# Kernel tuning notes

Hardware: AMD Instinct MI355X
Metric: run time of the kernel (lower is better)

The kernel has to match this reference:

```python
import jax, jax.numpy as jnp
import numpy as np

B, Q, K, D = 8, 2048, 2048, 64

def setup_inputs() -> dict:
    key = jax.random.key(0)
    kq, kk, kv, kl = jax.random.split(key, 4)
    queries = jax.random.normal(kq, (B, Q, D), dtype=jnp.float32)
    keys = jax.random.normal(kk, (B, K, D), dtype=jnp.float32)
    values = jax.random.normal(kv, (B, K, D), dtype=jnp.float32)
    valid_lens = jax.random.randint(kl, (B,), 1, K + 1)  # at least 1 valid key
    return {"queries": queries, "keys": keys, "values": values, "valid_lens": valid_lens}

def reference(queries, keys, values, valid_lens):
    d = queries.shape[-1]
    # scores: [B, Q, K]
    scores = jnp.einsum("bqd,bkd->bqk", queries, keys) / jnp.sqrt(jnp.float32(d))
    # d2l-style masked softmax: positions >= valid_len get -1e6 before softmax
    kpos = jnp.arange(scores.shape[-1])  # [K]
    mask = kpos[None, None, :] < valid_lens[:, None, None]  # [B,1,K]
    scores = jnp.where(mask, scores, jnp.float32(-1e6))
    attn = jax.nn.softmax(scores, axis=-1)
    # dropout is identity at inference (training=False)
    return jnp.einsum("bqk,bkd->bqd", attn, values)
```

## Files before the change

### kernel.cpp

```cpp
#include <hip/hip_runtime.h>

typedef float    f32x4  __attribute__((ext_vector_type(4)));
typedef float    f32x16 __attribute__((ext_vector_type(16)));
typedef _Float16 half8  __attribute__((ext_vector_type(8)));

constexpr int NB = 8;
constexpr int NQ = 2048;
constexpr int NKEY = 2048;
constexpr int DD = 64;
constexpr int KB = 64;

#define QSCALE (0.125f * 1.44269504088896340736f)

__device__ inline unsigned pkh(float a, float b) {
    return __builtin_bit_cast(unsigned, __builtin_amdgcn_cvt_pkrtz(a, b));
}
__device__ inline int vswz(int d) {
    return (((d >> 3) & 3) | ((d & 1) << 2)) << 4;
}

__device__ __forceinline__ void pv_chunk(
    const f32x16& sv, const char* __restrict__ vsm, int koff,
    int hi, int ql, int swzq, f32x16& o0, f32x16& o1)
{
    const unsigned w0 = pkh(sv[0],  sv[1]),  w1 = pkh(sv[2],  sv[3]);
    const unsigned w2 = pkh(sv[4],  sv[5]),  w3 = pkh(sv[6],  sv[7]);
    const unsigned w4 = pkh(sv[8],  sv[9]),  w5 = pkh(sv[10], sv[11]);
    const unsigned w6 = pkh(sv[12], sv[13]), w7 = pkh(sv[14], sv[15]);
    const unsigned p0 = __shfl_xor(w0, 32), p1 = __shfl_xor(w1, 32);
    const unsigned p2 = __shfl_xor(w2, 32), p3 = __shfl_xor(w3, 32);
    const unsigned p4 = __shfl_xor(w4, 32), p5 = __shfl_xor(w5, 32);
    const unsigned p6 = __shfl_xor(w6, 32), p7 = __shfl_xor(w7, 32);
    const bool h1 = (hi != 0);
    union { unsigned u[4]; half8 h; } A0, A1;
    A0.u[0] = h1 ? p2 : w0;  A0.u[1] = h1 ? p3 : w1;
    A0.u[2] = h1 ? w2 : p0;  A0.u[3] = h1 ? w3 : p1;
    A1.u[0] = h1 ? p6 : w4;  A1.u[1] = h1 ? p7 : w5;
    A1.u[2] = h1 ? w6 : p4;  A1.u[3] = h1 ? w7 : p5;

#pragma unroll
    for (int t = 0; t < 2; ++t) {
        const int co = koff + t * 32 + hi * 16;
        const half8 vb0 = *(const half8*)(vsm + ql * 128        + (co ^ swzq));
        const half8 vb1 = *(const half8*)(vsm + (32 + ql) * 128 + (co ^ swzq));
        const half8 pa = (t == 0) ? A0.h : A1.h;
        o0 = __builtin_amdgcn_mfma_f32_32x32x16_f16(pa, vb0, o0, 0, 0, 0);
        o1 = __builtin_amdgcn_mfma_f32_32x32x16_f16(pa, vb1, o1, 0, 0, 0);
    }
}

__global__ __launch_bounds__(256, 2) void attn_fused(
    const float* __restrict__ Qp, const float* __restrict__ Kp,
    const float* __restrict__ Vp, const int* __restrict__ VL,
    float* __restrict__ Op)
{
    __shared__ __align__(16) char pool[65536];

    const int tid  = threadIdx.x;
    const int wv   = tid >> 6;
    const int lane = tid & 63;
    const int ql   = lane & 31;
    const int hi   = lane >> 5;

    char* Ksm = pool + wv * 16384;
    char* Vsm = Ksm + 8192;

    const int b  = blockIdx.x & 7;
    const int qt = blockIdx.x >> 3;
    const int qbase = qt * 32;

    const int vlen = VL[b];
    const int numt = (vlen + KB - 1) / KB;

    const float* qsrc = Qp + ((size_t)b * NQ + qbase + ql) * DD;
    half8 qf[4];
#pragma unroll
    for (int c = 0; c < 4; ++c) {
        f32x4 f0 = *(const f32x4*)(qsrc + c * 16 + hi * 8);
        f32x4 f1 = *(const f32x4*)(qsrc + c * 16 + hi * 8 + 4);
        half8 h;
#pragma unroll
        for (int j = 0; j < 4; ++j) {
            h[j]     = (_Float16)(f0[j] * QSCALE);
            h[4 + j] = (_Float16)(f1[j] * QSCALE);
        }
        qf[c] = h;
    }

    f32x16 o0 = {}, o1 = {};
    float mrun = -1e30f, lrun = 0.f;

    const int kr_ = lane >> 3;
    const int kd0 = (lane & 7) * 8;
    const int vk2 = (lane >> 4) * 2;
    const int vd0 = (lane & 15) * 4;
    const int swzq = vswz(ql);

    for (int t = wv; t < numt; t += 4) {
        const int kbase = t * KB;
        const float* kbp = Kp + ((size_t)b * NKEY + kbase) * DD;
        const float* vbp = Vp + ((size_t)b * NKEY + kbase) * DD;

        f32x4 ka[8][2];
#pragma unroll
        for (int i = 0; i < 8; ++i) {
            const float* src = kbp + (size_t)(i * 8 + kr_) * DD + kd0;
            ka[i][0] = *(const f32x4*)src;
            ka[i][1] = *(const f32x4*)(src + 4);
        }
        f32x4 va[8][2];
#pragma unroll
        for (int i = 0; i < 8; ++i) {
            const float* src = vbp + (size_t)(i * 8 + vk2) * DD + vd0;
            va[i][0] = *(const f32x4*)src;
            va[i][1] = *(const f32x4*)(src + DD);
        }

#pragma unroll
        for (int i = 0; i < 8; ++i) {
            half8 h;
#pragma unroll
            for (int j = 0; j < 4; ++j) {
                h[j]     = (_Float16)ka[i][0][j];
                h[4 + j] = (_Float16)ka[i][1][j];
            }
            const int off = ((i * 8 + kr_) * 128 + kd0 * 2) ^ (kr_ << 4);
            *(half8*)(Ksm + off) = h;
        }

        f32x16 svA = {}, svB = {};
#pragma unroll
        for (int c = 0; c < 4; ++c) {
            const half8 kfA = *(const half8*)(Ksm +
                ((ql * 128 + c * 32 + hi * 16) ^ ((ql & 7) << 4)));
            svA = __builtin_amdgcn_mfma_f32_32x32x16_f16(kfA, qf[c], svA, 0, 0, 0);
            const half8 kfB = *(const half8*)(Ksm +
                (((32 + ql) * 128 + c * 32 + hi * 16) ^ ((ql & 7) << 4)));
            svB = __builtin_amdgcn_mfma_f32_32x32x16_f16(kfB, qf[c], svB, 0, 0, 0);
        }

#pragma unroll
        for (int i = 0; i < 8; ++i) {
#pragma unroll
            for (int jj = 0; jj < 4; ++jj) {
                const int d = vd0 + jj;
                const unsigned w = pkh(va[i][0][jj], va[i][1][jj]);
                *(unsigned*)(Vsm + d * 128 + (((i * 16 + vk2 * 2)) ^ vswz(d))) = w;
            }
        }

        if (kbase + KB > vlen) {
#pragma unroll
            for (int r = 0; r < 16; ++r) {
                const int krow = (r & 3) + 8 * (r >> 2) + 4 * hi;
                svA[r] = (kbase + krow < vlen)      ? svA[r] : -1e30f;
                svB[r] = (kbase + 32 + krow < vlen) ? svB[r] : -1e30f;
            }
        }

        float mx[16];
#pragma unroll
        for (int r = 0; r < 16; ++r) mx[r] = fmaxf(svA[r], svB[r]);
#pragma unroll
        for (int st = 8; st > 0; st >>= 1)
#pragma unroll
            for (int r = 0; r < st; ++r) mx[r] = fmaxf(mx[r], mx[r + st]);
        float mr = fmaxf(mx[0], __shfl_xor(mx[0], 32));

        if (!__all(mr <= mrun + 8.f)) {
            const float mn = fmaxf(mrun, mr);
            const float alpha = __builtin_amdgcn_exp2f(mrun - mn);
            lrun *= alpha;
            mrun = mn;
#pragma unroll
            for (int r = 0; r < 16; ++r) {
                const int qr = (r & 3) + 8 * (r >> 2) + 4 * hi;
                const float ar = __shfl(alpha, qr);
                o0[r] *= ar;
                o1[r] *= ar;
            }
        }

#pragma unroll
        for (int r = 0; r < 16; ++r) {
            svA[r] = __builtin_amdgcn_exp2f(svA[r] - mrun);
            svB[r] = __builtin_amdgcn_exp2f(svB[r] - mrun);
        }
        float sx[16];
#pragma unroll
        for (int r = 0; r < 16; ++r) sx[r] = svA[r] + svB[r];
#pragma unroll
        for (int st = 8; st > 0; st >>= 1)
#pragma unroll
            for (int r = 0; r < st; ++r) sx[r] += sx[r + st];
        lrun += sx[0] + __shfl_xor(sx[0], 32);

        pv_chunk(svA, Vsm, 0,  hi, ql, swzq, o0, o1);
        pv_chunk(svB, Vsm, 64, hi, ql, swzq, o0, o1);
    }

    __syncthreads();
    float* Mb = (float*)(pool + 32768);
    float* Lb = (float*)(pool + 32768 + 512);
    float* Tb = (float*)(pool + 32768 + 1024);
    float (*Obuf)[32][64] = (float (*)[32][64])pool;

    if (hi == 0) { Mb[wv * 32 + ql] = mrun; Lb[wv * 32 + ql] = lrun; }
    __syncthreads();

    float Mtot = -1e30f;
#pragma unroll
    for (int w = 0; w < 4; ++w)
        if (Lb[w * 32 + ql] > 0.f) Mtot = fmaxf(Mtot, Mb[w * 32 + ql]);
    float Ltot = 0.f;
#pragma unroll
    for (int w = 0; w < 4; ++w) {
        const float lw = Lb[w * 32 + ql];
        if (lw > 0.f) Ltot += lw * __builtin_amdgcn_exp2f(Mb[w * 32 + ql] - Mtot);
    }
    const float wown = (lrun > 0.f) ? __builtin_amdgcn_exp2f(mrun - Mtot) : 0.f;
    if (wv == 0 && hi == 0) Tb[ql] = Ltot;

#pragma unroll
    for (int r = 0; r < 16; ++r) {
        const int qr = (r & 3) + 8 * (r >> 2) + 4 * hi;
        const float wr = __shfl(wown, qr);
        Obuf[wv][qr][ql]      = o0[r] * wr;
        Obuf[wv][qr][ql + 32] = o1[r] * wr;
    }
    __syncthreads();

#pragma unroll
    for (int k = 0; k < 8; ++k) {
        const int q = wv * 8 + k;
        const float sum = Obuf[0][q][lane] + Obuf[1][q][lane]
                        + Obuf[2][q][lane] + Obuf[3][q][lane];
        Op[((size_t)b * NQ + qbase + q) * DD + lane] = sum / Tb[q];
    }
}

extern "C" void kernel_launch(void* const* d_in, const int* in_sizes, int n_in,
                              void* d_out, int out_size, void* d_ws, size_t ws_size,
                              hipStream_t stream) {
    const float* Qp = (const float*)d_in[0];
    const float* Kp = (const float*)d_in[1];
    const float* Vp = (const float*)d_in[2];
    const int*   VL = (const int*)d_in[3];
    float* Op = (float*)d_out;

    dim3 block(256);
    dim3 grid(NB * (NQ / 32));
    hipLaunchKernelGGL(attn_fused, grid, block, 0, stream, Qp, Kp, Vp, VL, Op);
}
```

Before: 30.29 us.

## Prefetch next K tile into registers, add MFMA priority, remap block-to-batch order

Restructures the per-wave key loop into a software pipeline. The next K tile (t+4) is loaded from global into a second register buffer while the current tile is converted and used, with the loop unrolled by two to ping-pong the buffers. It also raises wave priority around the MFMA sections with s_setprio, and changes the blockIdx mapping so neighbouring blocks interleave batches in groups of 8. The aim is to hide global load latency and improve MFMA issue. The risk is higher register pressure from the extra 32-float buffer, which could cause spills or reduce occupancy under launch_bounds(256,2).

```diff
diff --git a/kernel.cpp b/kernel.cpp
--- a/kernel.cpp
+++ b/kernel.cpp
@@ -38,6 +38,7 @@
     A1.u[0] = h1 ? p6 : w4;  A1.u[1] = h1 ? p7 : w5;
     A1.u[2] = h1 ? w6 : p4;  A1.u[3] = h1 ? w7 : p5;
 
+    __builtin_amdgcn_s_setprio(1);
 #pragma unroll
     for (int t = 0; t < 2; ++t) {
         const int co = koff + t * 32 + hi * 16;
@@ -47,6 +48,125 @@
         o0 = __builtin_amdgcn_mfma_f32_32x32x16_f16(pa, vb0, o0, 0, 0, 0);
         o1 = __builtin_amdgcn_mfma_f32_32x32x16_f16(pa, vb1, o1, 0, 0, 0);
     }
+    __builtin_amdgcn_s_setprio(0);
+}
+
+__device__ __forceinline__ void load_k(
+    f32x4 (&ka)[8][2], const float* __restrict__ kbp, int kr_, int kd0)
+{
+#pragma unroll
+    for (int i = 0; i < 8; ++i) {
+        const float* src = kbp + (size_t)(i * 8 + kr_) * DD + kd0;
+        ka[i][0] = *(const f32x4*)src;
+        ka[i][1] = *(const f32x4*)(src + 4);
+    }
+}
+
+__device__ __forceinline__ void iter_body(
+    f32x4 (&ka)[8][2], f32x4 (&kan)[8][2],
+    int t, int numt, int vlen, int b,
+    const float* __restrict__ Kp, const float* __restrict__ Vp,
+    char* __restrict__ Ksm, char* __restrict__ Vsm,
+    int ql, int hi, int kr_, int kd0, int vk2, int vd0, int swzq,
+    const half8 (&qf)[4], f32x16& o0, f32x16& o1, float& mrun, float& lrun)
+{
+    const int kbase = t * KB;
+
+    f32x4 va[8][2];
+    const float* vbp = Vp + ((size_t)b * NKEY + kbase) * DD;
+#pragma unroll
+    for (int i = 0; i < 8; ++i) {
+        const float* src = vbp + (size_t)(i * 8 + vk2) * DD + vd0;
+        va[i][0] = *(const f32x4*)src;
+        va[i][1] = *(const f32x4*)(src + DD);
+    }
+
+#pragma unroll
+    for (int i = 0; i < 8; ++i) {
+        half8 h;
+#pragma unroll
+        for (int j = 0; j < 4; ++j) {
+            h[j]     = (_Float16)ka[i][0][j];
+            h[4 + j] = (_Float16)ka[i][1][j];
+        }
+        const int off = ((i * 8 + kr_) * 128 + kd0 * 2) ^ (kr_ << 4);
+        *(half8*)(Ksm + off) = h;
+    }
+
+    if (t + 4 < numt)
+        load_k(kan, Kp + ((size_t)b * NKEY + (t + 4) * KB) * DD, kr_, kd0);
+
+    f32x16 svA = {}, svB = {};
+    __builtin_amdgcn_s_setprio(1);
+#pragma unroll
+    for (int c = 0; c < 4; ++c) {
+        const half8 kfA = *(const half8*)(Ksm +
+            ((ql * 128 + c * 32 + hi * 16) ^ ((ql & 7) << 4)));
+        svA = __builtin_amdgcn_mfma_f32_32x32x16_f16(kfA, qf[c], svA, 0, 0, 0);
+        const half8 kfB = *(const half8*)(Ksm +
+            (((32 + ql) * 128 + c * 32 + hi * 16) ^ ((ql & 7) << 4)));
+        svB = __builtin_amdgcn_mfma_f32_32x32x16_f16(kfB, qf[c], svB, 0, 0, 0);
+    }
+    __builtin_amdgcn_s_setprio(0);
+
+#pragma unroll
+    for (int i = 0; i < 8; ++i) {
+#pragma unroll
+        for (int jj = 0; jj < 4; ++jj) {
+            const int d = vd0 + jj;
+            const unsigned w = pkh(va[i][0][jj], va[i][1][jj]);
+            *(unsigned*)(Vsm + d * 128 + ((i * 16 + vk2 * 2) ^ vswz(d))) = w;
+        }
+    }
+
+    if (kbase + KB > vlen) {
+#pragma unroll
+        for (int r = 0; r < 16; ++r) {
+            const int krow = (r & 3) + 8 * (r >> 2) + 4 * hi;
+            svA[r] = (kbase + krow < vlen)      ? svA[r] : -1e30f;
+            svB[r] = (kbase + 32 + krow < vlen) ? svB[r] : -1e30f;
+        }
+    }
+
+    float mx[16];
+#pragma unroll
+    for (int r = 0; r < 16; ++r) mx[r] = fmaxf(svA[r], svB[r]);
+#pragma unroll
+    for (int st = 8; st > 0; st >>= 1)
+#pragma unroll
+        for (int r = 0; r < st; ++r) mx[r] = fmaxf(mx[r], mx[r + st]);
+    float mr = fmaxf(mx[0], __shfl_xor(mx[0], 32));
+
+    if (!__all(mr <= mrun + 8.f)) {
+        const float mn = fmaxf(mrun, mr);
+        const float alpha = __builtin_amdgcn_exp2f(mrun - mn);
+        lrun *= alpha;
+        mrun = mn;
+#pragma unroll
+        for (int r = 0; r < 16; ++r) {
+            const int qr = (r & 3) + 8 * (r >> 2) + 4 * hi;
+            const float ar = __shfl(alpha, qr);
+            o0[r] *= ar;
+            o1[r] *= ar;
+        }
+    }
+
+#pragma unroll
+    for (int r = 0; r < 16; ++r) {
+        svA[r] = __builtin_amdgcn_exp2f(svA[r] - mrun);
+        svB[r] = __builtin_amdgcn_exp2f(svB[r] - mrun);
+    }
+    float sx[16];
+#pragma unroll
+    for (int r = 0; r < 16; ++r) sx[r] = svA[r] + svB[r];
+#pragma unroll
+    for (int st = 8; st > 0; st >>= 1)
+#pragma unroll
+        for (int r = 0; r < st; ++r) sx[r] += sx[r + st];
+    lrun += sx[0] + __shfl_xor(sx[0], 32);
+
+    pv_chunk(svA, Vsm, 0,  hi, ql, swzq, o0, o1);
+    pv_chunk(svB, Vsm, 64, hi, ql, swzq, o0, o1);
 }
 
 __global__ __launch_bounds__(256, 2) void attn_fused(
@@ -65,8 +185,9 @@
     char* Ksm = pool + wv * 16384;
     char* Vsm = Ksm + 8192;
 
-    const int b  = blockIdx.x & 7;
-    const int qt = blockIdx.x >> 3;
+    const int g  = blockIdx.x;
+    const int b  = (g >> 3) & 7;
+    const int qt = ((g >> 6) << 3) | (g & 7);
     const int qbase = qt * 32;
 
     const int vlen = VL[b];
@@ -96,107 +217,18 @@
     const int vd0 = (lane & 15) * 4;
     const int swzq = vswz(ql);
 
-    for (int t = wv; t < numt; t += 4) {
-        const int kbase = t * KB;
-        const float* kbp = Kp + ((size_t)b * NKEY + kbase) * DD;
-        const float* vbp = Vp + ((size_t)b * NKEY + kbase) * DD;
-
-        f32x4 ka[8][2];
-#pragma unroll
-        for (int i = 0; i < 8; ++i) {
-            const float* src = kbp + (size_t)(i * 8 + kr_) * DD + kd0;
-            ka[i][0] = *(const f32x4*)src;
-            ka[i][1] = *(const f32x4*)(src + 4);
-        }
-        f32x4 va[8][2];
-#pragma unroll
-        for (int i = 0; i < 8; ++i) {
-            const float* src = vbp + (size_t)(i * 8 + vk2) * DD + vd0;
-            va[i][0] = *(const f32x4*)src;
-            va[i][1] = *(const f32x4*)(src + DD);
-        }
-
-#pragma unroll
-        for (int i = 0; i < 8; ++i) {
-            half8 h;
-#pragma unroll
-            for (int j = 0; j < 4; ++j) {
-                h[j]     = (_Float16)ka[i][0][j];
-                h[4 + j] = (_Float16)ka[i][1][j];
-            }
-            const int off = ((i * 8 + kr_) * 128 + kd0 * 2) ^ (kr_ << 4);
-            *(half8*)(Ksm + off) = h;
-        }
-
-        f32x16 svA = {}, svB = {};
-#pragma unroll
-        for (int c = 0; c < 4; ++c) {
-            const half8 kfA = *(const half8*)(Ksm +
-                ((ql * 128 + c * 32 + hi * 16) ^ ((ql & 7) << 4)));
-            svA = __builtin_amdgcn_mfma_f32_32x32x16_f16(kfA, qf[c], svA, 0, 0, 0);
-            const half8 kfB = *(const half8*)(Ksm +
-                (((32 + ql) * 128 + c * 32 + hi * 16) ^ ((ql & 7) << 4)));
-            svB = __builtin_amdgcn_mfma_f32_32x32x16_f16(kfB, qf[c], svB, 0, 0, 0);
-        }
-
-#pragma unroll
-        for (int i = 0; i < 8; ++i) {
-#pragma unroll
-            for (int jj = 0; jj < 4; ++jj) {
-                const int d = vd0 + jj;
-                const unsigned w = pkh(va[i][0][jj], va[i][1][jj]);
-                *(unsigned*)(Vsm + d * 128 + (((i * 16 + vk2 * 2)) ^ vswz(d))) = w;
-            }
-        }
-
-        if (kbase + KB > vlen) {
-#pragma unroll
-            for (int r = 0; r < 16; ++r) {
-                const int krow = (r & 3) + 8 * (r >> 2) + 4 * hi;
-                svA[r] = (kbase + krow < vlen)      ? svA[r] : -1e30f;
-                svB[r] = (kbase + 32 + krow < vlen) ? svB[r] : -1e30f;
-            }
-        }
-
-        float mx[16];
-#pragma unroll
-        for (int r = 0; r < 16; ++r) mx[r] = fmaxf(svA[r], svB[r]);
-#pragma unroll
-        for (int st = 8; st > 0; st >>= 1)
-#pragma unroll
-            for (int r = 0; r < st; ++r) mx[r] = fmaxf(mx[r], mx[r + st]);
-        float mr = fmaxf(mx[0], __shfl_xor(mx[0], 32));
-
-        if (!__all(mr <= mrun + 8.f)) {
-            const float mn = fmaxf(mrun, mr);
-            const float alpha = __builtin_amdgcn_exp2f(mrun - mn);
-            lrun *= alpha;
-            mrun = mn;
-#pragma unroll
-            for (int r = 0; r < 16; ++r) {
-                const int qr = (r & 3) + 8 * (r >> 2) + 4 * hi;
-                const float ar = __shfl(alpha, qr);
-                o0[r] *= ar;
-                o1[r] *= ar;
-            }
-        }
-
-#pragma unroll
-        for (int r = 0; r < 16; ++r) {
-            svA[r] = __builtin_amdgcn_exp2f(svA[r] - mrun);
-            svB[r] = __builtin_amdgcn_exp2f(svB[r] - mrun);
-        }
-        float sx[16];
-#pragma unroll
-        for (int r = 0; r < 16; ++r) sx[r] = svA[r] + svB[r];
-#pragma unroll
-        for (int st = 8; st > 0; st >>= 1)
-#pragma unroll
-            for (int r = 0; r < st; ++r) sx[r] += sx[r + st];
-        lrun += sx[0] + __shfl_xor(sx[0], 32);
-
-        pv_chunk(svA, Vsm, 0,  hi, ql, swzq, o0, o1);
-        pv_chunk(svB, Vsm, 64, hi, ql, swzq, o0, o1);
+    f32x4 kaA[8][2], kaB[8][2];
+    int t = wv;
+    if (t < numt)
+        load_k(kaA, Kp + ((size_t)b * NKEY + t * KB) * DD, kr_, kd0);
+    while (t < numt) {
+        iter_body(kaA, kaB, t, numt, vlen, b, Kp, Vp, Ksm, Vsm,
+                  ql, hi, kr_, kd0, vk2, vd0, swzq, qf, o0, o1, mrun, lrun);
+        t += 4;
+        if (t >= numt) break;
+        iter_body(kaB, kaA, t, numt, vlen, b, Kp, Vp, Ksm, Vsm,
+                  ql, hi, kr_, kd0, vk2, vd0, swzq, qf, o0, o1, mrun, lrun);
+        t += 4;
     }
 
     __syncthreads();
```

New measurement: 76.82 us. 154% more time.
